# Kernel tuning notes

Hardware: AMD Instinct MI355X
Metric: run time of the kernel (lower is better)

## Reference

```python
import jax, jax.numpy as jnp
import numpy as np


def setup_inputs() -> dict:
    key = jax.random.key(0)
    k1, k2 = jax.random.split(key)
    A, B, N, M, K = 8, 16, 1024, 1024, 64
    u = jax.random.normal(k1, (A, B, N, K), dtype=jnp.float32)
    v = jax.random.normal(k2, (A, B, M, K), dtype=jnp.float32)
    return {"u": u, "v": v}


def reference(u, v):
    # to_norm = u @ v^T has shape (A,B,N,M); we only need its row/col sums.
    # sum over M of (u @ v^T) = u @ sum_m(v);  sum over N = v @ sum_n(u).
    v_sum = v.sum(axis=2)                     # (A,B,K)
    u_sum = u.sum(axis=2)                     # (A,B,K)
    row_sum = jnp.einsum('abnk,abk->abn', u, v_sum)   # to_norm.sum(dim=3)
    col_sum = jnp.einsum('abmk,abk->abm', v, u_sum)   # to_norm.sum(dim=2)
    left_mul = jax.nn.relu(jnp.sign(row_sum))[..., None]   # (A,B,N,1)
    right_mul = jax.nn.relu(jnp.sign(col_sum))[..., None]  # (A,B,M,1)
    return (left_mul * u, right_mul * v)
```

## Files before the change

kernel.cpp:

```cpp
#include <hip/hip_runtime.h>


#define NBATCH 128
#define NROW   1024
#define KDIM   64
#define ELEMS_PER_TENSOR (128ull * 1024ull * 64ull)

typedef float floatx4 __attribute__((ext_vector_type(4)));

__global__ __launch_bounds__(1024)
void fused_local_kernel(const float* __restrict__ u,
                        const float* __restrict__ v,
                        float* __restrict__ out) {
    const int bid   = blockIdx.x;
    const int xcd   = bid & 7;
    const int slot  = bid >> 3;
    const int batch = xcd * 16 + (slot >> 1);
    const int half  = slot & 1;
    const int tid   = threadIdx.x;
    const int k4    = tid & 15;
    const int rg    = tid >> 4;
    const int wave  = tid >> 6;

    const float4* ub = (const float4*)(u + (size_t)batch * NROW * KDIM);
    const float4* vb = (const float4*)(v + (size_t)batch * NROW * KDIM);

    const int r_own0 = half * 512 + rg;
    const int r_oth0 = (1 - half) * 512 + rg;

    float4 ur[8], vr[8];
    float4 su = make_float4(0.f, 0.f, 0.f, 0.f);
    float4 sv = make_float4(0.f, 0.f, 0.f, 0.f);
    #pragma unroll
    for (int i = 0; i < 8; ++i) {
        size_t io = (size_t)(r_own0 + 64 * i) * 16 + k4;
        ur[i] = ub[io];
        vr[i] = vb[io];
        su.x += ur[i].x; su.y += ur[i].y; su.z += ur[i].z; su.w += ur[i].w;
        sv.x += vr[i].x; sv.y += vr[i].y; sv.z += vr[i].z; sv.w += vr[i].w;
    }
    #pragma unroll
    for (int i = 0; i < 8; ++i) {
        size_t ix = (size_t)(r_oth0 + 64 * i) * 16 + k4;
        float4 a = ub[ix];
        float4 b = vb[ix];
        su.x += a.x; su.y += a.y; su.z += a.z; su.w += a.w;
        sv.x += b.x; sv.y += b.y; sv.z += b.z; sv.w += b.w;
    }

    su.x += __shfl_xor(su.x, 16); su.y += __shfl_xor(su.y, 16);
    su.z += __shfl_xor(su.z, 16); su.w += __shfl_xor(su.w, 16);
    su.x += __shfl_xor(su.x, 32); su.y += __shfl_xor(su.y, 32);
    su.z += __shfl_xor(su.z, 32); su.w += __shfl_xor(su.w, 32);
    sv.x += __shfl_xor(sv.x, 16); sv.y += __shfl_xor(sv.y, 16);
    sv.z += __shfl_xor(sv.z, 16); sv.w += __shfl_xor(sv.w, 16);
    sv.x += __shfl_xor(sv.x, 32); sv.y += __shfl_xor(sv.y, 32);
    sv.z += __shfl_xor(sv.z, 32); sv.w += __shfl_xor(sv.w, 32);

    __shared__ float4 red_u[16][16];
    __shared__ float4 red_v[16][16];
    __shared__ float4 fsum[2][16];
    if ((tid & 63) < 16) {
        red_u[wave][k4] = su;
        red_v[wave][k4] = sv;
    }
    __syncthreads();

    if (tid < 32) {
        const int which = tid >> 4;
        const int c     = tid & 15;
        float4 t = make_float4(0.f, 0.f, 0.f, 0.f);
        if (which == 0) {
            #pragma unroll
            for (int i = 0; i < 16; ++i) {
                float4 b = red_v[i][c];
                t.x += b.x; t.y += b.y; t.z += b.z; t.w += b.w;
            }
        } else {
            #pragma unroll
            for (int i = 0; i < 16; ++i) {
                float4 a = red_u[i][c];
                t.x += a.x; t.y += a.y; t.z += a.z; t.w += a.w;
            }
        }
        fsum[which][c] = t;
    }
    __syncthreads();

    const float4 vs = fsum[0][k4];
    const float4 us = fsum[1][k4];

    float* ou = out + (size_t)batch * NROW * KDIM;
    float* ov = out + ELEMS_PER_TENSOR + (size_t)batch * NROW * KDIM;

    #pragma unroll
    for (int i = 0; i < 8; ++i) {
        size_t io = (size_t)(r_own0 + 64 * i) * 16 + k4;

        float pu = ur[i].x * vs.x + ur[i].y * vs.y + ur[i].z * vs.z + ur[i].w * vs.w;
        pu += __shfl_xor(pu, 1);
        pu += __shfl_xor(pu, 2);
        pu += __shfl_xor(pu, 4);
        pu += __shfl_xor(pu, 8);
        float mu = (pu > 0.f) ? 1.f : 0.f;
        floatx4 outu = { ur[i].x * mu, ur[i].y * mu, ur[i].z * mu, ur[i].w * mu };
        __builtin_nontemporal_store(outu, (floatx4*)(ou + io * 4));

        float pv = vr[i].x * us.x + vr[i].y * us.y + vr[i].z * us.z + vr[i].w * us.w;
        pv += __shfl_xor(pv, 1);
        pv += __shfl_xor(pv, 2);
        pv += __shfl_xor(pv, 4);
        pv += __shfl_xor(pv, 8);
        float mv = (pv > 0.f) ? 1.f : 0.f;
        floatx4 outv = { vr[i].x * mv, vr[i].y * mv, vr[i].z * mv, vr[i].w * mv };
        __builtin_nontemporal_store(outv, (floatx4*)(ov + io * 4));
    }
}

extern "C" void kernel_launch(void* const* d_in, const int* in_sizes, int n_in,
                              void* d_out, int out_size, void* d_ws, size_t ws_size,
                              hipStream_t stream) {
    const float* u = (const float*)d_in[0];
    const float* v = (const float*)d_in[1];
    float* out = (float*)d_out;

    fused_local_kernel<<<dim3(256), dim3(1024), 0, stream>>>(u, v, out);
}
```

Measured before the change: 114.1 us.

## Exchange half-batch partial sums between paired blocks via workspace flags

Each batch's two blocks now compute column sums only over their own half of the rows and swap the partials through a global workspace, using a release/acquire flag counter. This removes the redundant second read of the other half of u and v, which doubled the input traffic. If the partner block does not signal within a spin limit, the block falls back to reading the other half itself. The scheme relies on the two blocks being co-resident, adds spin-wait latency, and relies on the workspace being available.

```diff
diff --git a/kernel.cpp b/kernel.cpp
--- a/kernel.cpp
+++ b/kernel.cpp
@@ -6,7 +6,208 @@
 #define KDIM   64
 #define ELEMS_PER_TENSOR (128ull * 1024ull * 64ull)
 
+#define WS_PAYLOAD_FLOATS (NBATCH * 2 * 2 * 64)
+#define WS_FLAGS (NBATCH * 2)
+#define WS_BYTES ((size_t)WS_PAYLOAD_FLOATS * 4 + (size_t)WS_FLAGS * 4)
+
+#define SPIN_LIMIT 65536u
+
 typedef float floatx4 __attribute__((ext_vector_type(4)));
+
+__global__ __launch_bounds__(1024)
+void fused_pair_kernel(const float* __restrict__ u,
+                       const float* __restrict__ v,
+                       float* __restrict__ out,
+                       float* __restrict__ wsf,
+                       unsigned int* __restrict__ flags) {
+    const int bid   = blockIdx.x;
+    const int xcd   = bid & 7;
+    const int slot  = bid >> 3;
+    const int batch = xcd * 16 + (slot >> 1);
+    const int half  = slot & 1;
+    const int tid   = threadIdx.x;
+    const int k4    = tid & 15;
+    const int rg    = tid >> 4;
+    const int wave  = tid >> 6;
+    const int my_slot  = batch * 2 + half;
+    const int oth_slot = batch * 2 + (1 - half);
+
+    unsigned int base = 0u;
+    if (tid == 0)
+        base = __hip_atomic_load(&flags[oth_slot], __ATOMIC_RELAXED,
+                                 __HIP_MEMORY_SCOPE_AGENT);
+    __syncthreads();
+
+    const float4* ub = (const float4*)(u + (size_t)batch * NROW * KDIM);
+    const float4* vb = (const float4*)(v + (size_t)batch * NROW * KDIM);
+
+    const int r_own0 = half * 512 + rg;
+
+    float4 ur[8], vr[8];
+    float4 su = make_float4(0.f, 0.f, 0.f, 0.f);
+    float4 sv = make_float4(0.f, 0.f, 0.f, 0.f);
+    #pragma unroll
+    for (int i = 0; i < 8; ++i) {
+        size_t io = (size_t)(r_own0 + 64 * i) * 16 + k4;
+        ur[i] = ub[io];
+        vr[i] = vb[io];
+        su.x += ur[i].x; su.y += ur[i].y; su.z += ur[i].z; su.w += ur[i].w;
+        sv.x += vr[i].x; sv.y += vr[i].y; sv.z += vr[i].z; sv.w += vr[i].w;
+    }
+
+    su.x += __shfl_xor(su.x, 16); su.y += __shfl_xor(su.y, 16);
+    su.z += __shfl_xor(su.z, 16); su.w += __shfl_xor(su.w, 16);
+    su.x += __shfl_xor(su.x, 32); su.y += __shfl_xor(su.y, 32);
+    su.z += __shfl_xor(su.z, 32); su.w += __shfl_xor(su.w, 32);
+    sv.x += __shfl_xor(sv.x, 16); sv.y += __shfl_xor(sv.y, 16);
+    sv.z += __shfl_xor(sv.z, 16); sv.w += __shfl_xor(sv.w, 16);
+    sv.x += __shfl_xor(sv.x, 32); sv.y += __shfl_xor(sv.y, 32);
+    sv.z += __shfl_xor(sv.z, 32); sv.w += __shfl_xor(sv.w, 32);
+
+    __shared__ float4 red_u[16][16];
+    __shared__ float4 red_v[16][16];
+    __shared__ float4 fsum_own[2][16];
+    __shared__ float4 fsum_oth[2][16];
+    __shared__ int sh_timeout;
+    if ((tid & 63) < 16) {
+        red_u[wave][k4] = su;
+        red_v[wave][k4] = sv;
+    }
+    __syncthreads();
+
+    if (tid < 32) {
+        const int which = tid >> 4;
+        const int c     = tid & 15;
+        float4 t = make_float4(0.f, 0.f, 0.f, 0.f);
+        if (which == 0) {
+            #pragma unroll
+            for (int i = 0; i < 16; ++i) {
+                float4 b = red_v[i][c];
+                t.x += b.x; t.y += b.y; t.z += b.z; t.w += b.w;
+            }
+        } else {
+            #pragma unroll
+            for (int i = 0; i < 16; ++i) {
+                float4 a = red_u[i][c];
+                t.x += a.x; t.y += a.y; t.z += a.z; t.w += a.w;
+            }
+        }
+        fsum_own[which][c] = t;
+        float* dst = wsf + ((size_t)my_slot * 2 + which) * 64 + c * 4;
+        __hip_atomic_store(dst + 0, t.x, __ATOMIC_RELAXED, __HIP_MEMORY_SCOPE_AGENT);
+        __hip_atomic_store(dst + 1, t.y, __ATOMIC_RELAXED, __HIP_MEMORY_SCOPE_AGENT);
+        __hip_atomic_store(dst + 2, t.z, __ATOMIC_RELAXED, __HIP_MEMORY_SCOPE_AGENT);
+        __hip_atomic_store(dst + 3, t.w, __ATOMIC_RELAXED, __HIP_MEMORY_SCOPE_AGENT);
+    }
+    __syncthreads();
+
+    if (tid == 0) {
+        __hip_atomic_fetch_add(&flags[my_slot], 1u, __ATOMIC_RELEASE,
+                               __HIP_MEMORY_SCOPE_AGENT);
+        unsigned int spins = 0;
+        int ok = 1;
+        while ((__hip_atomic_load(&flags[oth_slot], __ATOMIC_ACQUIRE,
+                                  __HIP_MEMORY_SCOPE_AGENT) - base) == 0u) {
+            if (++spins > SPIN_LIMIT) { ok = 0; break; }
+        }
+        sh_timeout = !ok;
+    }
+    __syncthreads();
+
+    if (!sh_timeout) {
+        if (tid < 32) {
+            const int which = tid >> 4;
+            const int c     = tid & 15;
+            const float* src = wsf + ((size_t)oth_slot * 2 + which) * 64 + c * 4;
+            float4 t;
+            t.x = __hip_atomic_load(src + 0, __ATOMIC_RELAXED, __HIP_MEMORY_SCOPE_AGENT);
+            t.y = __hip_atomic_load(src + 1, __ATOMIC_RELAXED, __HIP_MEMORY_SCOPE_AGENT);
+            t.z = __hip_atomic_load(src + 2, __ATOMIC_RELAXED, __HIP_MEMORY_SCOPE_AGENT);
+            t.w = __hip_atomic_load(src + 3, __ATOMIC_RELAXED, __HIP_MEMORY_SCOPE_AGENT);
+            fsum_oth[which][c] = t;
+        }
+    } else {
+        const int r_oth0 = (1 - half) * 512 + rg;
+        float4 su2 = make_float4(0.f, 0.f, 0.f, 0.f);
+        float4 sv2 = make_float4(0.f, 0.f, 0.f, 0.f);
+        #pragma unroll
+        for (int i = 0; i < 8; ++i) {
+            size_t ix = (size_t)(r_oth0 + 64 * i) * 16 + k4;
+            float4 a = ub[ix];
+            float4 b = vb[ix];
+            su2.x += a.x; su2.y += a.y; su2.z += a.z; su2.w += a.w;
+            sv2.x += b.x; sv2.y += b.y; sv2.z += b.z; sv2.w += b.w;
+        }
+        su2.x += __shfl_xor(su2.x, 16); su2.y += __shfl_xor(su2.y, 16);
+        su2.z += __shfl_xor(su2.z, 16); su2.w += __shfl_xor(su2.w, 16);
+        su2.x += __shfl_xor(su2.x, 32); su2.y += __shfl_xor(su2.y, 32);
+        su2.z += __shfl_xor(su2.z, 32); su2.w += __shfl_xor(su2.w, 32);
+        sv2.x += __shfl_xor(sv2.x, 16); sv2.y += __shfl_xor(sv2.y, 16);
+        sv2.z += __shfl_xor(sv2.z, 16); sv2.w += __shfl_xor(sv2.w, 16);
+        sv2.x += __shfl_xor(sv2.x, 32); sv2.y += __shfl_xor(sv2.y, 32);
+        sv2.z += __shfl_xor(sv2.z, 32); sv2.w += __shfl_xor(sv2.w, 32);
+        if ((tid & 63) < 16) {
+            red_u[wave][k4] = su2;
+            red_v[wave][k4] = sv2;
+        }
+        __syncthreads();
+        if (tid < 32) {
+            const int which = tid >> 4;
+            const int c     = tid & 15;
+            float4 t = make_float4(0.f, 0.f, 0.f, 0.f);
+            if (which == 0) {
+                #pragma unroll
+                for (int i = 0; i < 16; ++i) {
+                    float4 b = red_v[i][c];
+                    t.x += b.x; t.y += b.y; t.z += b.z; t.w += b.w;
+                }
+            } else {
+                #pragma unroll
+                for (int i = 0; i < 16; ++i) {
+                    float4 a = red_u[i][c];
+                    t.x += a.x; t.y += a.y; t.z += a.z; t.w += a.w;
+                }
+            }
+            fsum_oth[which][c] = t;
+        }
+    }
+    __syncthreads();
+
+    const float4 vs = make_float4(fsum_own[0][k4].x + fsum_oth[0][k4].x,
+                                  fsum_own[0][k4].y + fsum_oth[0][k4].y,
+                                  fsum_own[0][k4].z + fsum_oth[0][k4].z,
+                                  fsum_own[0][k4].w + fsum_oth[0][k4].w);
+    const float4 us = make_float4(fsum_own[1][k4].x + fsum_oth[1][k4].x,
+                                  fsum_own[1][k4].y + fsum_oth[1][k4].y,
+                                  fsum_own[1][k4].z + fsum_oth[1][k4].z,
+                                  fsum_own[1][k4].w + fsum_oth[1][k4].w);
+
+    float* ou = out + (size_t)batch * NROW * KDIM;
+    float* ov = out + ELEMS_PER_TENSOR + (size_t)batch * NROW * KDIM;
+
+    #pragma unroll
+    for (int i = 0; i < 8; ++i) {
+        size_t io = (size_t)(r_own0 + 64 * i) * 16 + k4;
+
+        float pu = ur[i].x * vs.x + ur[i].y * vs.y + ur[i].z * vs.z + ur[i].w * vs.w;
+        pu += __shfl_xor(pu, 1);
+        pu += __shfl_xor(pu, 2);
+        pu += __shfl_xor(pu, 4);
+        pu += __shfl_xor(pu, 8);
+        float mu = (pu > 0.f) ? 1.f : 0.f;
+        floatx4 outu = { ur[i].x * mu, ur[i].y * mu, ur[i].z * mu, ur[i].w * mu };
+        __builtin_nontemporal_store(outu, (floatx4*)(ou + io * 4));
+
+        float pv = vr[i].x * us.x + vr[i].y * us.y + vr[i].z * us.z + vr[i].w * us.w;
+        pv += __shfl_xor(pv, 1);
+        pv += __shfl_xor(pv, 2);
+        pv += __shfl_xor(pv, 4);
+        pv += __shfl_xor(pv, 8);
+        float mv = (pv > 0.f) ? 1.f : 0.f;
+        floatx4 outv = { vr[i].x * mv, vr[i].y * mv, vr[i].z * mv, vr[i].w * mv };
+        __builtin_nontemporal_store(outv, (floatx4*)(ov + io * 4));
+    }
+}
 
 __global__ __launch_bounds__(1024)
 void fused_local_kernel(const float* __restrict__ u,
@@ -124,5 +325,11 @@
     const float* v = (const float*)d_in[1];
     float* out = (float*)d_out;
 
-    fused_local_kernel<<<dim3(256), dim3(1024), 0, stream>>>(u, v, out);
+    if (d_ws != nullptr && ws_size >= WS_BYTES) {
+        float* wsf = (float*)d_ws;
+        unsigned int* flags = (unsigned int*)((char*)d_ws + (size_t)WS_PAYLOAD_FLOATS * 4);
+        fused_pair_kernel<<<dim3(256), dim3(1024), 0, stream>>>(u, v, out, wsf, flags);
+    } else {
+        fused_local_kernel<<<dim3(256), dim3(1024), 0, stream>>>(u, v, out);
+    }
 }
```

After: 116.1 us. Within noise of the previous version (+1.7%).

## Stage v-sum reduction first so u outputs stream while u-sum accumulates

Applied to the files above, without the earlier changes.

The kernel now reduces v first, broadcasts the v column sum, and then loads u once. Each u row is masked and stored immediately while the u sum is accumulated in the same pass, so u output stores overlap with the remaining loads. The separate single-wave final reduction and one barrier are replaced by every thread reading the shared partials directly. This cuts register pressure (no held ur array) but serialises the v and u load phases, which may reduce memory-level parallelism.

```diff
diff --git a/kernel.cpp b/kernel.cpp
--- a/kernel.cpp
+++ b/kernel.cpp
@@ -9,9 +9,9 @@
 typedef float floatx4 __attribute__((ext_vector_type(4)));
 
 __global__ __launch_bounds__(1024)
-void fused_local_kernel(const float* __restrict__ u,
-                        const float* __restrict__ v,
-                        float* __restrict__ out) {
+void fused_overlap_kernel(const float* __restrict__ u,
+                          const float* __restrict__ v,
+                          float* __restrict__ out) {
     const int bid   = blockIdx.x;
     const int xcd   = bid & 7;
     const int slot  = bid >> 3;
@@ -22,90 +22,88 @@
     const int rg    = tid >> 4;
     const int wave  = tid >> 6;
 
-    const float4* ub = (const float4*)(u + (size_t)batch * NROW * KDIM);
-    const float4* vb = (const float4*)(v + (size_t)batch * NROW * KDIM);
+    const size_t boff = (size_t)batch * NROW * KDIM;
+    const float4* ub = (const float4*)(u + boff);
+    const float4* vb = (const float4*)(v + boff);
+    float* ou = out + boff;
+    float* ov = out + ELEMS_PER_TENSOR + boff;
 
     const int r_own0 = half * 512 + rg;
     const int r_oth0 = (1 - half) * 512 + rg;
 
-    float4 ur[8], vr[8];
-    float4 su = make_float4(0.f, 0.f, 0.f, 0.f);
+    __shared__ float4 red_v[16][16];
+    __shared__ float4 red_u[16][16];
+
+    float4 vr[8];
     float4 sv = make_float4(0.f, 0.f, 0.f, 0.f);
     #pragma unroll
     for (int i = 0; i < 8; ++i) {
         size_t io = (size_t)(r_own0 + 64 * i) * 16 + k4;
-        ur[i] = ub[io];
         vr[i] = vb[io];
-        su.x += ur[i].x; su.y += ur[i].y; su.z += ur[i].z; su.w += ur[i].w;
         sv.x += vr[i].x; sv.y += vr[i].y; sv.z += vr[i].z; sv.w += vr[i].w;
     }
     #pragma unroll
     for (int i = 0; i < 8; ++i) {
         size_t ix = (size_t)(r_oth0 + 64 * i) * 16 + k4;
+        float4 b = vb[ix];
+        sv.x += b.x; sv.y += b.y; sv.z += b.z; sv.w += b.w;
+    }
+
+    sv.x += __shfl_xor(sv.x, 16); sv.y += __shfl_xor(sv.y, 16);
+    sv.z += __shfl_xor(sv.z, 16); sv.w += __shfl_xor(sv.w, 16);
+    sv.x += __shfl_xor(sv.x, 32); sv.y += __shfl_xor(sv.y, 32);
+    sv.z += __shfl_xor(sv.z, 32); sv.w += __shfl_xor(sv.w, 32);
+    if ((tid & 63) < 16)
+        red_v[wave][k4] = sv;
+    __syncthreads();
+
+    float4 vs = make_float4(0.f, 0.f, 0.f, 0.f);
+    #pragma unroll
+    for (int w = 0; w < 16; ++w) {
+        float4 t = red_v[w][k4];
+        vs.x += t.x; vs.y += t.y; vs.z += t.z; vs.w += t.w;
+    }
+
+    float4 su = make_float4(0.f, 0.f, 0.f, 0.f);
+    #pragma unroll
+    for (int i = 0; i < 8; ++i) {
+        size_t io = (size_t)(r_own0 + 64 * i) * 16 + k4;
+        float4 a = ub[io];
+        su.x += a.x; su.y += a.y; su.z += a.z; su.w += a.w;
+        float pu = a.x * vs.x + a.y * vs.y + a.z * vs.z + a.w * vs.w;
+        pu += __shfl_xor(pu, 1);
+        pu += __shfl_xor(pu, 2);
+        pu += __shfl_xor(pu, 4);
+        pu += __shfl_xor(pu, 8);
+        float mu = (pu > 0.f) ? 1.f : 0.f;
+        floatx4 outu = { a.x * mu, a.y * mu, a.z * mu, a.w * mu };
+        __builtin_nontemporal_store(outu, (floatx4*)(ou + io * 4));
+    }
+    #pragma unroll
+    for (int i = 0; i < 8; ++i) {
+        size_t ix = (size_t)(r_oth0 + 64 * i) * 16 + k4;
         float4 a = ub[ix];
-        float4 b = vb[ix];
         su.x += a.x; su.y += a.y; su.z += a.z; su.w += a.w;
-        sv.x += b.x; sv.y += b.y; sv.z += b.z; sv.w += b.w;
     }
 
     su.x += __shfl_xor(su.x, 16); su.y += __shfl_xor(su.y, 16);
     su.z += __shfl_xor(su.z, 16); su.w += __shfl_xor(su.w, 16);
     su.x += __shfl_xor(su.x, 32); su.y += __shfl_xor(su.y, 32);
     su.z += __shfl_xor(su.z, 32); su.w += __shfl_xor(su.w, 32);
-    sv.x += __shfl_xor(sv.x, 16); sv.y += __shfl_xor(sv.y, 16);
-    sv.z += __shfl_xor(sv.z, 16); sv.w += __shfl_xor(sv.w, 16);
-    sv.x += __shfl_xor(sv.x, 32); sv.y += __shfl_xor(sv.y, 32);
-    sv.z += __shfl_xor(sv.z, 32); sv.w += __shfl_xor(sv.w, 32);
-
-    __shared__ float4 red_u[16][16];
-    __shared__ float4 red_v[16][16];
-    __shared__ float4 fsum[2][16];
-    if ((tid & 63) < 16) {
+    if ((tid & 63) < 16)
         red_u[wave][k4] = su;
-        red_v[wave][k4] = sv;
-    }
     __syncthreads();
 
-    if (tid < 32) {
-        const int which = tid >> 4;
-        const int c     = tid & 15;
-        float4 t = make_float4(0.f, 0.f, 0.f, 0.f);
-        if (which == 0) {
-            #pragma unroll
-            for (int i = 0; i < 16; ++i) {
-                float4 b = red_v[i][c];
-                t.x += b.x; t.y += b.y; t.z += b.z; t.w += b.w;
-            }
-        } else {
-            #pragma unroll
-            for (int i = 0; i < 16; ++i) {
-                float4 a = red_u[i][c];
-                t.x += a.x; t.y += a.y; t.z += a.z; t.w += a.w;
-            }
-        }
-        fsum[which][c] = t;
+    float4 us = make_float4(0.f, 0.f, 0.f, 0.f);
+    #pragma unroll
+    for (int w = 0; w < 16; ++w) {
+        float4 t = red_u[w][k4];
+        us.x += t.x; us.y += t.y; us.z += t.z; us.w += t.w;
     }
-    __syncthreads();
-
-    const float4 vs = fsum[0][k4];
-    const float4 us = fsum[1][k4];
-
-    float* ou = out + (size_t)batch * NROW * KDIM;
-    float* ov = out + ELEMS_PER_TENSOR + (size_t)batch * NROW * KDIM;
 
     #pragma unroll
     for (int i = 0; i < 8; ++i) {
         size_t io = (size_t)(r_own0 + 64 * i) * 16 + k4;
-
-        float pu = ur[i].x * vs.x + ur[i].y * vs.y + ur[i].z * vs.z + ur[i].w * vs.w;
-        pu += __shfl_xor(pu, 1);
-        pu += __shfl_xor(pu, 2);
-        pu += __shfl_xor(pu, 4);
-        pu += __shfl_xor(pu, 8);
-        float mu = (pu > 0.f) ? 1.f : 0.f;
-        floatx4 outu = { ur[i].x * mu, ur[i].y * mu, ur[i].z * mu, ur[i].w * mu };
-        __builtin_nontemporal_store(outu, (floatx4*)(ou + io * 4));
-
         float pv = vr[i].x * us.x + vr[i].y * us.y + vr[i].z * us.z + vr[i].w * us.w;
         pv += __shfl_xor(pv, 1);
         pv += __shfl_xor(pv, 2);
@@ -124,5 +122,5 @@
     const float* v = (const float*)d_in[1];
     float* out = (float*)d_out;
 
-    fused_local_kernel<<<dim3(256), dim3(1024), 0, stream>>>(u, v, out);
+    fused_overlap_kernel<<<dim3(256), dim3(1024), 0, stream>>>(u, v, out);
 }
```

New measurement: 117.9 us. 3.3% more time.
